# Kernel tuning notes

Hardware: AMD Instinct MI355X
Metric: run time of the kernel (lower is better)

## Reference

```python
import jax, jax.numpy as jnp
import numpy as np


def setup_inputs() -> dict:
    key = jax.random.key(0)
    k1, k2, k3 = jax.random.split(key, 3)
    B, T, D = 8, 4096, 1024
    x0 = jax.random.normal(k1, (B, D), dtype=jnp.float32)
    a = jax.random.uniform(k2, (B, T, D), dtype=jnp.float32)  # decay in [0,1) for stability
    u = jax.random.normal(k3, (B, T, D), dtype=jnp.float32)
    return {"x0": x0, "a": a, "u": u}


def _linear_scan(x0, a, u):
    # x_t = a_t * x_{t-1} + u_t, t = 1..T (x_0 given)
    # Fold x0 into the first step so the associative scan handles it uniformly.
    u0 = u.at[:, 0, :].add(a[:, 0, :] * x0)

    def combine(c1, c2):
        a1, u1 = c1
        a2, u2 = c2
        return a1 * a2, a2 * u1 + u2

    _, x = jax.lax.associative_scan(combine, (a, u0), axis=1)
    return x  # [B, T, D]


def reference(x0, a, u):
    return _linear_scan(x0, a, u)
```

## Files before the change

kernel.cpp:

```cpp
#include <hip/hip_runtime.h>

#define BB 8
#define TT 4096
#define DD 1024
#define SS 128
#define TSEG (TT / SS)
#define STR2 (DD / 2)
#define CH 4
#define NB (TSEG / CH)

typedef float natf2 __attribute__((ext_vector_type(2)));

#define GLOAD2(dst, ptr) \
  asm volatile("global_load_dwordx2 %0, %1, off" : "=v"(dst) : "v"(ptr))
#define GSTORE2(ptr, val) \
  asm volatile("global_store_dwordx2 %0, %1, off" ::"v"(ptr), "v"(val) : "memory")
#define SWAITV(n) asm volatile("s_waitcnt vmcnt(" #n ")" ::: "memory")
#define KEEP(v) asm volatile("" ::"v"(v))

__global__ __launch_bounds__(512) void seg_reduce(
    const float* __restrict__ a, const float* __restrict__ u,
    float* __restrict__ wsA, float* __restrict__ wsU) {
  const int b = blockIdx.x >> 7;
  const int s = blockIdx.x & (SS - 1);
  const int d2 = threadIdx.x << 1;

  const size_t base = ((size_t)b * TT + (size_t)s * TSEG) * DD + d2;
  const natf2* __restrict__ ap = (const natf2*)(a + base);
  const natf2* __restrict__ up = (const natf2*)(u + base);

  natf2 av[2][CH], uv[2][CH];
#pragma unroll
  for (int k = 0; k < CH; ++k) {
    GLOAD2(av[0][k], ap + (size_t)k * STR2);
    GLOAD2(uv[0][k], up + (size_t)k * STR2);
  }

  natf2 A = {1.f, 1.f};
  natf2 U = {0.f, 0.f};

#pragma unroll
  for (int i = 0; i < NB; ++i) {
    const int pb = i & 1;
    if (i + 1 < NB) {
#pragma unroll
      for (int k = 0; k < CH; ++k) {
        GLOAD2(av[pb ^ 1][k], ap + (size_t)((i + 1) * CH + k) * STR2);
        GLOAD2(uv[pb ^ 1][k], up + (size_t)((i + 1) * CH + k) * STR2);
      }
      SWAITV(8);
    } else {
      SWAITV(0);
    }
    __builtin_amdgcn_sched_barrier(0);
#pragma unroll
    for (int k = 0; k < CH; ++k) {
      const natf2 a2 = av[pb][k], u2 = uv[pb][k];
      U.x = fmaf(a2.x, U.x, u2.x);
      U.y = fmaf(a2.y, U.y, u2.y);
      A.x *= a2.x;
      A.y *= a2.y;
    }
  }

  const size_t w = ((size_t)b * SS + s) * DD + d2;
  *(natf2*)(wsA + w) = A;
  *(natf2*)(wsU + w) = U;
}

__global__ __launch_bounds__(256) void seg_scan(
    const float* __restrict__ x0, const float* __restrict__ wsA,
    const float* __restrict__ wsU, float* __restrict__ xstart) {
  __shared__ float ldsA[SS * 64];
  __shared__ float ldsU[SS * 64];
  __shared__ float wsumA[4][64];
  __shared__ float wsumU[4][64];

  const int b  = blockIdx.x >> 4;
  const int d0 = (blockIdx.x & 15) << 6;
  const int ch = threadIdx.x & 63;
  const int wv = threadIdx.x >> 6;

#pragma unroll 8
  for (int it = 0; it < SS / 4; ++it) {
    const int s = (it << 2) + wv;
    const size_t g = ((size_t)b * SS + s) * DD + d0 + ch;
    ldsA[s * 64 + ch] = wsA[g];
    ldsU[s * 64 + ch] = wsU[g];
  }
  __syncthreads();

  float Ac = 1.f, Uc = 0.f;
  const int s0 = wv * (SS / 4);
#pragma unroll 8
  for (int k = 0; k < SS / 4; ++k) {
    const float As = ldsA[(s0 + k) * 64 + ch];
    const float Us = ldsU[(s0 + k) * 64 + ch];
    Uc = fmaf(As, Uc, Us);
    Ac *= As;
  }
  wsumA[wv][ch] = Ac;
  wsumU[wv][ch] = Uc;
  __syncthreads();

  float x = x0[(size_t)b * DD + d0 + ch];
  for (int w2 = 0; w2 < wv; ++w2)
    x = fmaf(wsumA[w2][ch], x, wsumU[w2][ch]);

#pragma unroll 8
  for (int k = 0; k < SS / 4; ++k) {
    const int s = s0 + k;
    xstart[((size_t)b * SS + s) * DD + d0 + ch] = x;
    x = fmaf(ldsA[s * 64 + ch], x, ldsU[s * 64 + ch]);
  }
}

__global__ __launch_bounds__(512) void seg_apply(
    const float* __restrict__ a, const float* __restrict__ u,
    const float* __restrict__ xstart, float* __restrict__ out) {
  const int b = blockIdx.x >> 7;
  const int s = blockIdx.x & (SS - 1);
  const int d2 = threadIdx.x << 1;

  const size_t base = ((size_t)b * TT + (size_t)s * TSEG) * DD + d2;
  const natf2* __restrict__ ap = (const natf2*)(a + base);
  const natf2* __restrict__ up = (const natf2*)(u + base);
  natf2* __restrict__ op = (natf2*)(out + base);

  const size_t w = ((size_t)b * SS + s) * DD + d2;
  natf2 x = *(const natf2*)(xstart + w);

  natf2 av[2][CH], uv[2][CH], sv[2][CH];
#pragma unroll
  for (int k = 0; k < CH; ++k) {
    GLOAD2(av[0][k], ap + (size_t)k * STR2);
    GLOAD2(uv[0][k], up + (size_t)k * STR2);
  }

#pragma unroll
  for (int i = 0; i < NB; ++i) {
    const int pb = i & 1;
    if (i + 1 < NB) {
#pragma unroll
      for (int k = 0; k < CH; ++k) {
        GLOAD2(av[pb ^ 1][k], ap + (size_t)((i + 1) * CH + k) * STR2);
        GLOAD2(uv[pb ^ 1][k], up + (size_t)((i + 1) * CH + k) * STR2);
      }
      if (i == 0) { SWAITV(8); } else { SWAITV(12); }
    } else {
      SWAITV(4);
    }
    __builtin_amdgcn_sched_barrier(0);
    if (i >= 2) {
#pragma unroll
      for (int k = 0; k < CH; ++k) KEEP(sv[pb][k]);
    }
#pragma unroll
    for (int k = 0; k < CH; ++k) {
      const natf2 a2 = av[pb][k], u2 = uv[pb][k];
      x.x = fmaf(a2.x, x.x, u2.x);
      x.y = fmaf(a2.y, x.y, u2.y);
      sv[pb][k] = x;
      GSTORE2(op + (size_t)(i * CH + k) * STR2, sv[pb][k]);
    }
  }
  SWAITV(0);
#pragma unroll
  for (int k = 0; k < CH; ++k) { KEEP(sv[0][k]); KEEP(sv[1][k]); }
}

extern "C" void kernel_launch(void* const* d_in, const int* in_sizes, int n_in,
                              void* d_out, int out_size, void* d_ws, size_t ws_size,
                              hipStream_t stream) {
  const float* x0 = (const float*)d_in[0];
  const float* a  = (const float*)d_in[1];
  const float* u  = (const float*)d_in[2];
  float* out = (float*)d_out;

  const size_t seg_elems = (size_t)BB * SS * DD;
  float* wsA    = (float*)d_ws;
  float* wsU    = wsA + seg_elems;
  float* xstart = wsU + seg_elems;

  seg_reduce<<<BB * SS, 512, 0, stream>>>(a, u, wsA, wsU);
  seg_scan<<<BB * (DD / 64), 256, 0, stream>>>(x0, wsA, wsU, xstart);
  seg_apply<<<BB * SS, 512, 0, stream>>>(a, u, xstart, out);
}
```

Before: 387.1 us.

## Stage a/u through LDS with async global_load_lds and two segments per block

Reduce and apply kernels now copy 8-row chunks of a and u straight from global memory into double-buffered shared memory using global_load_lds, and read operands back from LDS. Each block handles two time segments (64 rows), which halves the grid and lengthens each block's streaming pipeline. The aim is deeper memory-level parallelism for this bandwidth-bound scan. It adds block-wide barriers and 128KB of LDS per block, which limits occupancy, and relies on hand-tuned vmcnt counts.

```diff
diff --git a/kernel.cpp b/kernel.cpp
--- a/kernel.cpp
+++ b/kernel.cpp
@@ -1,71 +1,95 @@
 #include <hip/hip_runtime.h>
+#include <stdint.h>
 
 #define BB 8
 #define TT 4096
 #define DD 1024
 #define SS 128
-#define TSEG (TT / SS)
-#define STR2 (DD / 2)
-#define CH 4
-#define NB (TSEG / CH)
+#define TSEG 32
+#define SPB 2
+#define ROWS (SPB * TSEG)
+#define CHR 8
+#define NCH (ROWS / CHR)
+#define GRID13 (BB * SS / SPB)
 
 typedef float natf2 __attribute__((ext_vector_type(2)));
-
+typedef const void __attribute__((address_space(1))) gvoid;
+typedef void __attribute__((address_space(3))) lvoid;
+
+#define SWAITV(n) asm volatile("s_waitcnt vmcnt(" #n ")" ::: "memory")
 #define GLOAD2(dst, ptr) \
   asm volatile("global_load_dwordx2 %0, %1, off" : "=v"(dst) : "v"(ptr))
 #define GSTORE2(ptr, val) \
   asm volatile("global_store_dwordx2 %0, %1, off" ::"v"(ptr), "v"(val) : "memory")
-#define SWAITV(n) asm volatile("s_waitcnt vmcnt(" #n ")" ::: "memory")
 #define KEEP(v) asm volatile("" ::"v"(v))
+
+static __device__ __forceinline__ void gload16(const float* g, float* l) {
+  __builtin_amdgcn_global_load_lds((gvoid*)g, (lvoid*)l, 16, 0, 0);
+}
 
 __global__ __launch_bounds__(512) void seg_reduce(
     const float* __restrict__ a, const float* __restrict__ u,
     float* __restrict__ wsA, float* __restrict__ wsU) {
-  const int b = blockIdx.x >> 7;
-  const int s = blockIdx.x & (SS - 1);
-  const int d2 = threadIdx.x << 1;
-
-  const size_t base = ((size_t)b * TT + (size_t)s * TSEG) * DD + d2;
-  const natf2* __restrict__ ap = (const natf2*)(a + base);
-  const natf2* __restrict__ up = (const natf2*)(u + base);
-
-  natf2 av[2][CH], uv[2][CH];
-#pragma unroll
-  for (int k = 0; k < CH; ++k) {
-    GLOAD2(av[0][k], ap + (size_t)k * STR2);
-    GLOAD2(uv[0][k], up + (size_t)k * STR2);
-  }
-
-  natf2 A = {1.f, 1.f};
-  natf2 U = {0.f, 0.f};
-
-#pragma unroll
-  for (int i = 0; i < NB; ++i) {
-    const int pb = i & 1;
-    if (i + 1 < NB) {
-#pragma unroll
-      for (int k = 0; k < CH; ++k) {
-        GLOAD2(av[pb ^ 1][k], ap + (size_t)((i + 1) * CH + k) * STR2);
-        GLOAD2(uv[pb ^ 1][k], up + (size_t)((i + 1) * CH + k) * STR2);
-      }
+  __shared__ float lds[2][2][CHR][DD];
+  const int tid = threadIdx.x;
+  const int b  = blockIdx.x >> 6;
+  const int sg = blockIdx.x & 63;
+  const int d2 = tid << 1;
+  const size_t row0 = (size_t)b * TT + (size_t)sg * ROWS;
+  const float* ga = a + row0 * DD;
+  const float* gu = u + row0 * DD;
+  const int mb = tid & ~63;
+
+#pragma unroll
+  for (int k = 0; k < 4; ++k)
+    gload16(ga + (size_t)((k * 512 + tid) << 2), &lds[0][0][0][0] + ((k * 512 + mb) << 2));
+#pragma unroll
+  for (int k = 0; k < 4; ++k)
+    gload16(gu + (size_t)((k * 512 + tid) << 2), &lds[0][1][0][0] + ((k * 512 + mb) << 2));
+
+  float A0x = 1.f, A0y = 1.f, U0x = 0.f, U0y = 0.f;
+  float A1x = 1.f, A1y = 1.f, U1x = 0.f, U1y = 0.f;
+
+#pragma unroll
+  for (int g = 0; g < NCH; ++g) {
+    __builtin_amdgcn_s_barrier();
+    if (g + 1 < NCH) {
+      const float* ca = ga + (size_t)(g + 1) * CHR * DD;
+      const float* cu = gu + (size_t)(g + 1) * CHR * DD;
+      float* la = &lds[(g + 1) & 1][0][0][0];
+      float* lu = &lds[(g + 1) & 1][1][0][0];
+#pragma unroll
+      for (int k = 0; k < 4; ++k)
+        gload16(ca + (size_t)((k * 512 + tid) << 2), la + ((k * 512 + mb) << 2));
+#pragma unroll
+      for (int k = 0; k < 4; ++k)
+        gload16(cu + (size_t)((k * 512 + tid) << 2), lu + ((k * 512 + mb) << 2));
       SWAITV(8);
     } else {
       SWAITV(0);
     }
+    __builtin_amdgcn_s_barrier();
     __builtin_amdgcn_sched_barrier(0);
 #pragma unroll
-    for (int k = 0; k < CH; ++k) {
-      const natf2 a2 = av[pb][k], u2 = uv[pb][k];
-      U.x = fmaf(a2.x, U.x, u2.x);
-      U.y = fmaf(a2.y, U.y, u2.y);
-      A.x *= a2.x;
-      A.y *= a2.y;
-    }
-  }
-
-  const size_t w = ((size_t)b * SS + s) * DD + d2;
-  *(natf2*)(wsA + w) = A;
-  *(natf2*)(wsU + w) = U;
+    for (int r = 0; r < CHR; ++r) {
+      const natf2 a2 = *(const natf2*)&lds[g & 1][0][r][d2];
+      const natf2 u2 = *(const natf2*)&lds[g & 1][1][r][d2];
+      if (g < NCH / 2) {
+        U0x = fmaf(a2.x, U0x, u2.x); U0y = fmaf(a2.y, U0y, u2.y);
+        A0x *= a2.x; A0y *= a2.y;
+      } else {
+        U1x = fmaf(a2.x, U1x, u2.x); U1y = fmaf(a2.y, U1y, u2.y);
+        A1x *= a2.x; A1y *= a2.y;
+      }
+    }
+  }
+
+  const size_t w0 = ((size_t)b * SS + (size_t)sg * SPB) * DD + d2;
+  natf2 t;
+  t.x = A0x; t.y = A0y; *(natf2*)(wsA + w0) = t;
+  t.x = U0x; t.y = U0y; *(natf2*)(wsU + w0) = t;
+  t.x = A1x; t.y = A1y; *(natf2*)(wsA + w0 + DD) = t;
+  t.x = U1x; t.y = U1y; *(natf2*)(wsU + w0 + DD) = t;
 }
 
 __global__ __launch_bounds__(256) void seg_scan(
@@ -118,55 +142,79 @@
 __global__ __launch_bounds__(512) void seg_apply(
     const float* __restrict__ a, const float* __restrict__ u,
     const float* __restrict__ xstart, float* __restrict__ out) {
-  const int b = blockIdx.x >> 7;
-  const int s = blockIdx.x & (SS - 1);
-  const int d2 = threadIdx.x << 1;
-
-  const size_t base = ((size_t)b * TT + (size_t)s * TSEG) * DD + d2;
-  const natf2* __restrict__ ap = (const natf2*)(a + base);
-  const natf2* __restrict__ up = (const natf2*)(u + base);
-  natf2* __restrict__ op = (natf2*)(out + base);
-
-  const size_t w = ((size_t)b * SS + s) * DD + d2;
-  natf2 x = *(const natf2*)(xstart + w);
-
-  natf2 av[2][CH], uv[2][CH], sv[2][CH];
-#pragma unroll
-  for (int k = 0; k < CH; ++k) {
-    GLOAD2(av[0][k], ap + (size_t)k * STR2);
-    GLOAD2(uv[0][k], up + (size_t)k * STR2);
-  }
-
-#pragma unroll
-  for (int i = 0; i < NB; ++i) {
-    const int pb = i & 1;
-    if (i + 1 < NB) {
-#pragma unroll
-      for (int k = 0; k < CH; ++k) {
-        GLOAD2(av[pb ^ 1][k], ap + (size_t)((i + 1) * CH + k) * STR2);
-        GLOAD2(uv[pb ^ 1][k], up + (size_t)((i + 1) * CH + k) * STR2);
+  __shared__ float lds[2][2][CHR][DD];
+  const int tid = threadIdx.x;
+  const int b  = blockIdx.x >> 6;
+  const int sg = blockIdx.x & 63;
+  const int d2 = tid << 1;
+  const size_t row0 = (size_t)b * TT + (size_t)sg * ROWS;
+  const float* ga = a + row0 * DD;
+  const float* gu = u + row0 * DD;
+  float* gout = out + row0 * DD;
+  const int mb = tid & ~63;
+
+  natf2 xs0, xs1;
+  const float* xp = xstart + ((size_t)b * SS + (size_t)sg * SPB) * DD + d2;
+  GLOAD2(xs0, xp);
+  GLOAD2(xs1, xp + DD);
+
+#pragma unroll
+  for (int k = 0; k < 4; ++k)
+    gload16(ga + (size_t)((k * 512 + tid) << 2), &lds[0][0][0][0] + ((k * 512 + mb) << 2));
+#pragma unroll
+  for (int k = 0; k < 4; ++k)
+    gload16(gu + (size_t)((k * 512 + tid) << 2), &lds[0][1][0][0] + ((k * 512 + mb) << 2));
+
+  natf2 x;
+  natf2 sv0[CHR], sv1[CHR];
+
+#pragma unroll
+  for (int g = 0; g < NCH; ++g) {
+    __builtin_amdgcn_s_barrier();
+    if (g + 1 < NCH) {
+      const float* ca = ga + (size_t)(g + 1) * CHR * DD;
+      const float* cu = gu + (size_t)(g + 1) * CHR * DD;
+      float* la = &lds[(g + 1) & 1][0][0][0];
+      float* lu = &lds[(g + 1) & 1][1][0][0];
+#pragma unroll
+      for (int k = 0; k < 4; ++k)
+        gload16(ca + (size_t)((k * 512 + tid) << 2), la + ((k * 512 + mb) << 2));
+#pragma unroll
+      for (int k = 0; k < 4; ++k)
+        gload16(cu + (size_t)((k * 512 + tid) << 2), lu + ((k * 512 + mb) << 2));
+      if (g == 0) { SWAITV(8); }
+      else        { SWAITV(16); }
+    } else {
+      SWAITV(8);
+    }
+    __builtin_amdgcn_s_barrier();
+    __builtin_amdgcn_sched_barrier(0);
+    if (g >= 2) {
+#pragma unroll
+      for (int r = 0; r < CHR; ++r) {
+        if (g & 1) KEEP(sv1[r]); else KEEP(sv0[r]);
       }
-      if (i == 0) { SWAITV(8); } else { SWAITV(12); }
-    } else {
-      SWAITV(4);
-    }
-    __builtin_amdgcn_sched_barrier(0);
-    if (i >= 2) {
-#pragma unroll
-      for (int k = 0; k < CH; ++k) KEEP(sv[pb][k]);
-    }
-#pragma unroll
-    for (int k = 0; k < CH; ++k) {
-      const natf2 a2 = av[pb][k], u2 = uv[pb][k];
+    }
+    if (g == 0) x = xs0;
+    if (g == NCH / 2) x = xs1;
+#pragma unroll
+    for (int r = 0; r < CHR; ++r) {
+      const natf2 a2 = *(const natf2*)&lds[g & 1][0][r][d2];
+      const natf2 u2 = *(const natf2*)&lds[g & 1][1][r][d2];
       x.x = fmaf(a2.x, x.x, u2.x);
       x.y = fmaf(a2.y, x.y, u2.y);
-      sv[pb][k] = x;
-      GSTORE2(op + (size_t)(i * CH + k) * STR2, sv[pb][k]);
+      if (g & 1) {
+        sv1[r] = x;
+        GSTORE2((natf2*)(gout + (size_t)(g * CHR + r) * DD + d2), sv1[r]);
+      } else {
+        sv0[r] = x;
+        GSTORE2((natf2*)(gout + (size_t)(g * CHR + r) * DD + d2), sv0[r]);
+      }
     }
   }
   SWAITV(0);
 #pragma unroll
-  for (int k = 0; k < CH; ++k) { KEEP(sv[0][k]); KEEP(sv[1][k]); }
+  for (int r = 0; r < CHR; ++r) { KEEP(sv0[r]); KEEP(sv1[r]); }
 }
 
 extern "C" void kernel_launch(void* const* d_in, const int* in_sizes, int n_in,
@@ -182,7 +230,7 @@
   float* wsU    = wsA + seg_elems;
   float* xstart = wsU + seg_elems;
 
-  seg_reduce<<<BB * SS, 512, 0, stream>>>(a, u, wsA, wsU);
+  seg_reduce<<<GRID13, 512, 0, stream>>>(a, u, wsA, wsU);
   seg_scan<<<BB * (DD / 64), 256, 0, stream>>>(x0, wsA, wsU, xstart);
-  seg_apply<<<BB * SS, 512, 0, stream>>>(a, u, xstart, out);
-}
+  seg_apply<<<GRID13, 512, 0, stream>>>(a, u, xstart, out);
+}
```

Result: faster. 372.4 us (-3.8%).
